# Optimization experiments

Measured on AMD Instinct MI355X. Metric: run time of the kernel, lower is better.

Reference implementation:

```python
import jax, jax.numpy as jnp
import numpy as np

B, S, D = 4, 2048, 1024
H = 16
HD = D // H

def setup_inputs() -> dict:
    key = jax.random.key(0)
    ks = jax.random.split(key, 6)
    scale = 1.0 / np.sqrt(D)
    x = jax.random.normal(ks[0], (B, S, D), dtype=jnp.float32)
    Wq = jax.random.normal(ks[1], (D, D), dtype=jnp.float32) * scale
    Wk = jax.random.normal(ks[2], (D, D), dtype=jnp.float32) * scale
    Wv = jax.random.normal(ks[3], (D, D), dtype=jnp.float32) * scale
    Wo = jax.random.normal(ks[4], (D, D), dtype=jnp.float32) * scale
    bo = jax.random.normal(ks[5], (D,), dtype=jnp.float32) * 0.01
    return {"x": x, "Wq": Wq, "Wk": Wk, "Wv": Wv, "Wo": Wo, "bo": bo}

def reference(x, Wq, Wk, Wv, Wo, bo):
    b, n, _ = x.shape
    # QKV projections (no bias), split into heads: [b, h, n, hd]
    q = (x @ Wq).reshape(b, n, H, HD).transpose(0, 2, 1, 3)
    k = (x @ Wk).reshape(b, n, H, HD).transpose(0, 2, 1, 3)
    v = (x @ Wv).reshape(b, n, H, HD).transpose(0, 2, 1, 3)
    scores = jnp.einsum('bhqd,bhkd->bhqk', q, k) / jnp.sqrt(jnp.float32(HD))
    causal = jnp.tril(jnp.ones((n, n), dtype=bool))
    scores = jnp.where(causal, scores, -jnp.inf)
    attn = jax.nn.softmax(scores, axis=-1)  # dropout p=0.0 -> identity
    ctx = jnp.einsum('bhqk,bhkd->bhqd', attn, v)
    ctx = ctx.transpose(0, 2, 1, 3).reshape(b, n, D)
    return ctx @ Wo + bo
```

## Files before the change

### kernel.cpp

```cpp
#include <hip/hip_runtime.h>

#define S_   2048
#define D_   1024
#define H_   16
#define HD_  64
#define NTOK 8192
#define QKS  2048
#define QSCALE 0.18033688f

typedef __attribute__((ext_vector_type(8))) __bf16 bf16x8;
typedef __attribute__((ext_vector_type(4))) __bf16 bf16x4;
typedef __attribute__((ext_vector_type(4))) float  f32x4;
typedef __attribute__((ext_vector_type(4))) short  short4v;

#define GPTR(p) ((__attribute__((address_space(1))) void*)(unsigned long long)(p))
#define LPTR(p) ((__attribute__((address_space(3))) void*)(p))

__global__ __launch_bounds__(256) void k_prep(const float* __restrict__ x,
                                              __bf16* __restrict__ xb,
                                              const float* __restrict__ Wq,
                                              const float* __restrict__ Wk,
                                              const float* __restrict__ Wv,
                                              const float* __restrict__ Wo,
                                              __bf16* __restrict__ wqkt,
                                              __bf16* __restrict__ wvt,
                                              __bf16* __restrict__ wot) {
    const int bx = blockIdx.x;
    if (bx < 4096) {
        int i = bx * 2048 + threadIdx.x * 8;
        f32x4 a = *(const f32x4*)(x + i);
        f32x4 b = *(const f32x4*)(x + i + 4);
        bf16x8 o;
#pragma unroll
        for (int j = 0; j < 4; j++) { o[j] = (__bf16)a[j]; o[4 + j] = (__bf16)b[j]; }
        *(bf16x8*)(xb + i) = o;
        return;
    }
    __shared__ float t[32][33];
    const int tt = bx - 4096;
    const int widx = tt >> 10, r = tt & 1023;
    const float* W;
    __bf16* Wt;
    switch (widx) {
        case 0: W = Wq; Wt = wqkt; break;
        case 1: W = Wk; Wt = wqkt + (size_t)D_ * D_; break;
        case 2: W = Wv; Wt = wvt; break;
        default: W = Wo; Wt = wot; break;
    }
    const int i0 = (r & 31) * 32, j0 = (r >> 5) * 32;
    const int tx = threadIdx.x & 31, ty = threadIdx.x >> 5;
#pragma unroll
    for (int rr = 0; rr < 32; rr += 8)
        t[ty + rr][tx] = W[(size_t)(i0 + ty + rr) * D_ + j0 + tx];
    __syncthreads();
#pragma unroll
    for (int rr = 0; rr < 32; rr += 8)
        Wt[(size_t)(j0 + ty + rr) * D_ + i0 + tx] = (__bf16)t[tx][ty + rr];
}

__device__ __forceinline__ void gemm_body_bf16(const __bf16* __restrict__ A,
                                               const __bf16* __restrict__ Bt,
                                               __bf16* __restrict__ C,
                                               int N, int K, int tm, int tn,
                                               float scale, int vperm,
                                               __bf16* As, __bf16* Bs) {
    const int tid  = threadIdx.x;
    const int wave = tid >> 6, lane = tid & 63;
    const int quad = lane >> 4, l16 = lane & 15;
    const int wm = (wave & 1) * 64, wn = (wave >> 1) * 64;
    f32x4 acc[4][4] = {};

    for (int k0 = 0; k0 < K; k0 += 32) {
        __syncthreads();
#pragma unroll
        for (int s = 0; s < 2; s++) {
            const int cb = s * 256 + wave * 64;
            const int c  = cb + lane;
            const int row = c >> 2;
            const int kc  = ((c & 3) ^ ((row >> 1) & 3)) * 8;
            __builtin_amdgcn_global_load_lds(GPTR(A + (size_t)(tm + row) * K + k0 + kc),
                                             LPTR(As + cb * 8), 16, 0, 0);
            __builtin_amdgcn_global_load_lds(GPTR(Bt + (size_t)(tn + row) * K + k0 + kc),
                                             LPTR(Bs + cb * 8), 16, 0, 0);
        }
        __syncthreads();

        bf16x8 af[4], bf[4];
#pragma unroll
        for (int mi = 0; mi < 4; mi++) {
            const int rf = wm + mi * 16 + l16;
            af[mi] = *(const bf16x8*)&As[rf * 32 + (quad ^ ((rf >> 1) & 3)) * 8];
        }
#pragma unroll
        for (int ni = 0; ni < 4; ni++) {
            const int rf = wn + ni * 16 + l16;
            bf[ni] = *(const bf16x8*)&Bs[rf * 32 + (quad ^ ((rf >> 1) & 3)) * 8];
        }
#pragma unroll
        for (int mi = 0; mi < 4; mi++)
#pragma unroll
            for (int ni = 0; ni < 4; ni++)
                acc[mi][ni] = __builtin_amdgcn_mfma_f32_16x16x32_bf16(
                    af[mi], bf[ni], acc[mi][ni], 0, 0, 0);
    }

#pragma unroll
    for (int mi = 0; mi < 4; mi++)
#pragma unroll
        for (int ni = 0; ni < 4; ni++)
#pragma unroll
            for (int r = 0; r < 4; r++) {
                const int row = tm + wm + mi * 16 + quad * 4 + r;
                const int col = tn + wn + ni * 16 + l16;
                const int xr  = (vperm & (row >> 3) & 1) << 2;
                C[(size_t)row * N + (col ^ xr)] = (__bf16)(acc[mi][ni][r] * scale);
            }
}

__global__ __launch_bounds__(256) void k_gemm_qkv(const __bf16* __restrict__ xb,
                                                  const __bf16* __restrict__ wqkt,
                                                  const __bf16* __restrict__ wvt,
                                                  __bf16* __restrict__ qk,
                                                  __bf16* __restrict__ VT) {
    __shared__ __bf16 As[128 * 32];
    __shared__ __bf16 Bs[128 * 32];
    const int bx = blockIdx.x;
    if (bx < 1024) {
        const int tm = (bx & 63) * 128, tn = (bx >> 6) * 128;
        const float scale = (tn < D_) ? QSCALE : 1.0f;
        gemm_body_bf16(xb, wqkt, qk, QKS, D_, tm, tn, scale, 0, As, Bs);
    } else {
        const int b2 = bx - 1024;
        const int tn = (b2 & 63) * 128, tm = (b2 >> 6) * 128;
        gemm_body_bf16(wvt, xb, VT, NTOK, D_, tm, tn, 1.0f, 1, As, Bs);
    }
}

__global__ __launch_bounds__(256) void k_gemm_o(const __bf16* __restrict__ A,
                                                const __bf16* __restrict__ Bt,
                                                float* __restrict__ C,
                                                const float* __restrict__ bias) {
    __shared__ __bf16 As[128 * 32];
    __shared__ __bf16 Bs[128 * 32];
    const int tid  = threadIdx.x;
    const int wave = tid >> 6, lane = tid & 63;
    const int quad = lane >> 4, l16 = lane & 15;
    const int tm = blockIdx.x * 128, tn = blockIdx.y * 128;
    const int wm = (wave & 1) * 64, wn = (wave >> 1) * 64;
    const int N = D_, K = D_;
    f32x4 acc[4][4] = {};

    for (int k0 = 0; k0 < K; k0 += 32) {
        __syncthreads();
#pragma unroll
        for (int s = 0; s < 2; s++) {
            const int cb = s * 256 + wave * 64;
            const int c  = cb + lane;
            const int row = c >> 2;
            const int kc  = ((c & 3) ^ ((row >> 1) & 3)) * 8;
            __builtin_amdgcn_global_load_lds(GPTR(A + (size_t)(tm + row) * K + k0 + kc),
                                             LPTR(As + cb * 8), 16, 0, 0);
            __builtin_amdgcn_global_load_lds(GPTR(Bt + (size_t)(tn + row) * K + k0 + kc),
                                             LPTR(Bs + cb * 8), 16, 0, 0);
        }
        __syncthreads();

        bf16x8 af[4], bf[4];
#pragma unroll
        for (int mi = 0; mi < 4; mi++) {
            const int rf = wm + mi * 16 + l16;
            af[mi] = *(const bf16x8*)&As[rf * 32 + (quad ^ ((rf >> 1) & 3)) * 8];
        }
#pragma unroll
        for (int ni = 0; ni < 4; ni++) {
            const int rf = wn + ni * 16 + l16;
            bf[ni] = *(const bf16x8*)&Bs[rf * 32 + (quad ^ ((rf >> 1) & 3)) * 8];
        }
#pragma unroll
        for (int mi = 0; mi < 4; mi++)
#pragma unroll
            for (int ni = 0; ni < 4; ni++)
                acc[mi][ni] = __builtin_amdgcn_mfma_f32_16x16x32_bf16(
                    af[mi], bf[ni], acc[mi][ni], 0, 0, 0);
    }

#pragma unroll
    for (int mi = 0; mi < 4; mi++)
#pragma unroll
        for (int ni = 0; ni < 4; ni++)
#pragma unroll
            for (int r = 0; r < 4; r++) {
                const int row = tm + wm + mi * 16 + quad * 4 + r;
                const int col = tn + wn + ni * 16 + l16;
                C[(size_t)row * N + col] = acc[mi][ni][r] + bias[col];
            }
}

__device__ __forceinline__ short bf16_bits(float f) {
    __bf16 h = (__bf16)f;
    return __builtin_bit_cast(short, h);
}

__global__ __launch_bounds__(256, 2) void k_attn(const __bf16* __restrict__ Qb,
                                                 const __bf16* __restrict__ Kb,
                                                 const __bf16* __restrict__ VT,
                                                 __bf16* __restrict__ ctx) {
    __shared__ __bf16 Ks[2][64 * 64];
    __shared__ __bf16 Vs[2][64 * 64];

    const int tid = threadIdx.x;
    const int wave = tid >> 6, lane = tid & 63;
    const int quad = lane >> 4, l16 = lane & 15;
    const int bid = blockIdx.x;
    const int hb  = ((bid >> 6) << 3) | (bid & 7);
    const int qp  = (bid >> 3) & 7;
    const int h = hb >> 2, b = hb & 3;
    const size_t tok0 = (size_t)b * S_;
    const size_t hoff = (size_t)h * HD_;

    auto stage = [&](int kv, int buf) {
#pragma unroll
        for (int s = 0; s < 2; s++) {
            const int cb = s * 256 + wave * 64;
            const int c  = cb + lane;
            const int row = c >> 3;
            const int gc  = (c & 7) ^ (row & 7);
            __builtin_amdgcn_global_load_lds(
                GPTR(Kb + (size_t)(tok0 + kv + row) * QKS + hoff + gc * 8),
                LPTR(&Ks[buf][cb * 8]), 16, 0, 0);
            __builtin_amdgcn_global_load_lds(
                GPTR(VT + (hoff + row) * (size_t)NTOK + tok0 + kv + gc * 8),
                LPTR(&Vs[buf][cb * 8]), 16, 0, 0);
        }
    };

#pragma unroll 1
    for (int sidx = 0; sidx < 2; sidx++) {
        const int qt = sidx == 0 ? qp : 15 - qp;
        const int qb = qt * 128;
        const int q0 = qb + wave * 32;

        bf16x8 qf[2][2];
#pragma unroll
        for (int qi = 0; qi < 2; qi++)
#pragma unroll
            for (int ks = 0; ks < 2; ks++)
                qf[qi][ks] = *(const bf16x8*)&Qb[(tok0 + q0 + qi * 16 + l16) * QKS +
                                                 hoff + ks * 32 + quad * 8];

        f32x4 oacc[2][4] = {};
        float lsum[2] = {0.f, 0.f};
        const int ktb = (qb + 127) >> 6;

        stage(0, 0);
        __syncthreads();

        for (int kt = 0; kt <= ktb; kt++) {
            const int cur = kt & 1;
            const int kv0 = kt * 64;
            if (kt < ktb) stage(kv0 + 64, 1 - cur);

            if (kv0 <= q0 + 31) {
                f32x4 st[2][4] = {};
#pragma unroll
                for (int ks = 0; ks < 2; ks++)
#pragma unroll
                    for (int ksub = 0; ksub < 4; ksub++) {
                        const int r = ksub * 16 + l16;
                        bf16x8 kf = *(const bf16x8*)
                            &Ks[cur][(r * 8 + (((ks * 4 + quad) ^ (r & 7)))) * 8];
#pragma unroll
                        for (int qi = 0; qi < 2; qi++)
                            st[qi][ksub] = __builtin_amdgcn_mfma_f32_16x16x32_bf16(
                                kf, qf[qi][ks], st[qi][ksub], 0, 0, 0);
                    }
                if (kv0 + 63 > q0) {
#pragma unroll
                    for (int qi = 0; qi < 2; qi++)
#pragma unroll
                        for (int ksub = 0; ksub < 4; ksub++)
#pragma unroll
                            for (int r = 0; r < 4; r++) {
                                const int kg = kv0 + ksub * 16 + quad * 4 + r;
                                const int qg = q0 + qi * 16 + l16;
                                if (kg > qg) st[qi][ksub][r] = -1e30f;
                            }
                }
                short4v pfrag[2][4];
#pragma unroll
                for (int qi = 0; qi < 2; qi++)
#pragma unroll
                    for (int ksub = 0; ksub < 4; ksub++) {
                        float p0 = __builtin_amdgcn_exp2f(st[qi][ksub][0]);
                        float p1 = __builtin_amdgcn_exp2f(st[qi][ksub][1]);
                        float p2 = __builtin_amdgcn_exp2f(st[qi][ksub][2]);
                        float p3 = __builtin_amdgcn_exp2f(st[qi][ksub][3]);
                        lsum[qi] += (p0 + p1) + (p2 + p3);
                        short4v pf = {bf16_bits(p0), bf16_bits(p1),
                                      bf16_bits(p2), bf16_bits(p3)};
                        pfrag[qi][ksub] = pf;
                    }
#pragma unroll
                for (int ksub = 0; ksub < 4; ksub++)
#pragma unroll
                    for (int hs = 0; hs < 4; hs++) {
                        const int row = hs * 16 + l16;
                        const int swz = (ksub * 2 + (quad >> 1)) ^ (row & 7);
                        short4v vf = *(const short4v*)
                            &Vs[cur][row * 64 + swz * 8 + ((quad ^ (l16 >> 3)) & 1) * 4];
#pragma unroll
                        for (int qi = 0; qi < 2; qi++)
                            oacc[qi][hs] = __builtin_amdgcn_mfma_f32_16x16x16bf16_1k(
                                vf, pfrag[qi][ksub], oacc[qi][hs], 0, 0, 0);
                    }
            }
            __syncthreads();
        }

#pragma unroll
        for (int qi = 0; qi < 2; qi++) {
            float v = lsum[qi];
            v += __shfl_xor(v, 16);
            v += __shfl_xor(v, 32);
            const float rl = 1.0f / v;
#pragma unroll
            for (int hs = 0; hs < 4; hs++) {
                bf16x4 o;
#pragma unroll
                for (int r = 0; r < 4; r++) o[r] = (__bf16)(oacc[qi][hs][r] * rl);
                *(bf16x4*)&ctx[(tok0 + q0 + qi * 16 + l16) * D_ + hoff +
                               hs * 16 + quad * 4] = o;
            }
        }
    }
}

extern "C" void kernel_launch(void* const* d_in, const int* in_sizes, int n_in,
                              void* d_out, int out_size, void* d_ws, size_t ws_size,
                              hipStream_t stream) {
    const float* x  = (const float*)d_in[0];
    const float* Wq = (const float*)d_in[1];
    const float* Wk = (const float*)d_in[2];
    const float* Wv = (const float*)d_in[3];
    const float* Wo = (const float*)d_in[4];
    const float* bo = (const float*)d_in[5];
    float* out = (float*)d_out;

    char* p = (char*)d_ws;
    __bf16* xb   = (__bf16*)p; p += (size_t)NTOK * D_ * 2;
    __bf16* wqkt = (__bf16*)p; p += (size_t)2 * D_ * D_ * 2;
    __bf16* wvt  = (__bf16*)p; p += (size_t)D_ * D_ * 2;
    __bf16* wot  = (__bf16*)p; p += (size_t)D_ * D_ * 2;
    __bf16* qk   = (__bf16*)p; p += (size_t)NTOK * QKS * 2;
    __bf16* VT   = (__bf16*)p; p += (size_t)NTOK * D_ * 2;
    __bf16* ctx  = (__bf16*)p; p += (size_t)NTOK * D_ * 2;

    k_prep<<<dim3(4096 + 4 * 1024), 256, 0, stream>>>(x, xb, Wq, Wk, Wv, Wo,
                                                      wqkt, wvt, wot);
    k_gemm_qkv<<<dim3(1024 + 512), 256, 0, stream>>>(xb, wqkt, wvt, qk, VT);
    k_attn<<<dim3(512), 256, 0, stream>>>(qk, qk + D_, VT, ctx);
    k_gemm_o<<<dim3(64, 8), 256, 0, stream>>>(ctx, wot, out, bo);
}
```

Baseline: 232.1 us.

## Shrink attention query tile to 64 rows and double grid with occupancy 4

```diff
diff --git a/kernel.cpp b/kernel.cpp
--- a/kernel.cpp
+++ b/kernel.cpp
@@ -201,7 +201,7 @@
     return __builtin_bit_cast(short, h);
 }
 
-__global__ __launch_bounds__(256, 2) void k_attn(const __bf16* __restrict__ Qb,
+__global__ __launch_bounds__(256, 4) void k_attn(const __bf16* __restrict__ Qb,
                                                  const __bf16* __restrict__ Kb,
                                                  const __bf16* __restrict__ VT,
                                                  __bf16* __restrict__ ctx) {
@@ -212,8 +212,8 @@
     const int wave = tid >> 6, lane = tid & 63;
     const int quad = lane >> 4, l16 = lane & 15;
     const int bid = blockIdx.x;
-    const int hb  = ((bid >> 6) << 3) | (bid & 7);
-    const int qp  = (bid >> 3) & 7;
+    const int hb  = ((bid >> 7) << 3) | (bid & 7);
+    const int qp  = (bid >> 3) & 15;
     const int h = hb >> 2, b = hb & 3;
     const size_t tok0 = (size_t)b * S_;
     const size_t hoff = (size_t)h * HD_;
@@ -235,22 +235,20 @@
     };
 
 #pragma unroll 1
-    for (int sidx = 0; sidx < 2; sidx++) {
-        const int qt = sidx == 0 ? qp : 15 - qp;
-        const int qb = qt * 128;
-        const int q0 = qb + wave * 32;
-
-        bf16x8 qf[2][2];
-#pragma unroll
-        for (int qi = 0; qi < 2; qi++)
-#pragma unroll
-            for (int ks = 0; ks < 2; ks++)
-                qf[qi][ks] = *(const bf16x8*)&Qb[(tok0 + q0 + qi * 16 + l16) * QKS +
-                                                 hoff + ks * 32 + quad * 8];
-
-        f32x4 oacc[2][4] = {};
-        float lsum[2] = {0.f, 0.f};
-        const int ktb = (qb + 127) >> 6;
+    for (int pass = 0; pass < 2; pass++) {
+        const int j  = pass == 0 ? 31 - qp : qp;
+        const int qb = j * 64;
+        const int q0 = qb + wave * 16;
+
+        bf16x8 qf[2];
+#pragma unroll
+        for (int ks = 0; ks < 2; ks++)
+            qf[ks] = *(const bf16x8*)&Qb[(tok0 + q0 + l16) * QKS +
+                                         hoff + ks * 32 + quad * 8];
+
+        f32x4 oacc[4] = {};
+        float lsum = 0.f;
+        const int ktb = j;
 
         stage(0, 0);
         __syncthreads();
@@ -260,8 +258,8 @@
             const int kv0 = kt * 64;
             if (kt < ktb) stage(kv0 + 64, 1 - cur);
 
-            if (kv0 <= q0 + 31) {
-                f32x4 st[2][4] = {};
+            if (kv0 <= q0 + 15) {
+                f32x4 st[4] = {};
 #pragma unroll
                 for (int ks = 0; ks < 2; ks++)
 #pragma unroll
@@ -269,37 +267,31 @@
                         const int r = ksub * 16 + l16;
                         bf16x8 kf = *(const bf16x8*)
                             &Ks[cur][(r * 8 + (((ks * 4 + quad) ^ (r & 7)))) * 8];
-#pragma unroll
-                        for (int qi = 0; qi < 2; qi++)
-                            st[qi][ksub] = __builtin_amdgcn_mfma_f32_16x16x32_bf16(
-                                kf, qf[qi][ks], st[qi][ksub], 0, 0, 0);
+                        st[ksub] = __builtin_amdgcn_mfma_f32_16x16x32_bf16(
+                            kf, qf[ks], st[ksub], 0, 0, 0);
                     }
                 if (kv0 + 63 > q0) {
 #pragma unroll
-                    for (int qi = 0; qi < 2; qi++)
-#pragma unroll
-                        for (int ksub = 0; ksub < 4; ksub++)
-#pragma unroll
-                            for (int r = 0; r < 4; r++) {
-                                const int kg = kv0 + ksub * 16 + quad * 4 + r;
-                                const int qg = q0 + qi * 16 + l16;
-                                if (kg > qg) st[qi][ksub][r] = -1e30f;
-                            }
+                    for (int ksub = 0; ksub < 4; ksub++)
+#pragma unroll
+                        for (int r = 0; r < 4; r++) {
+                            const int kg = kv0 + ksub * 16 + quad * 4 + r;
+                            const int qg = q0 + l16;
+                            if (kg > qg) st[ksub][r] = -1e30f;
+                        }
                 }
-                short4v pfrag[2][4];
-#pragma unroll
-                for (int qi = 0; qi < 2; qi++)
-#pragma unroll
-                    for (int ksub = 0; ksub < 4; ksub++) {
-                        float p0 = __builtin_amdgcn_exp2f(st[qi][ksub][0]);
-                        float p1 = __builtin_amdgcn_exp2f(st[qi][ksub][1]);
-                        float p2 = __builtin_amdgcn_exp2f(st[qi][ksub][2]);
-                        float p3 = __builtin_amdgcn_exp2f(st[qi][ksub][3]);
-                        lsum[qi] += (p0 + p1) + (p2 + p3);
-                        short4v pf = {bf16_bits(p0), bf16_bits(p1),
-                                      bf16_bits(p2), bf16_bits(p3)};
-                        pfrag[qi][ksub] = pf;
-                    }
+                short4v pfrag[4];
+#pragma unroll
+                for (int ksub = 0; ksub < 4; ksub++) {
+                    float p0 = __builtin_amdgcn_exp2f(st[ksub][0]);
+                    float p1 = __builtin_amdgcn_exp2f(st[ksub][1]);
+                    float p2 = __builtin_amdgcn_exp2f(st[ksub][2]);
+                    float p3 = __builtin_amdgcn_exp2f(st[ksub][3]);
+                    lsum += (p0 + p1) + (p2 + p3);
+                    short4v pf = {bf16_bits(p0), bf16_bits(p1),
+                                  bf16_bits(p2), bf16_bits(p3)};
+                    pfrag[ksub] = pf;
+                }
 #pragma unroll
                 for (int ksub = 0; ksub < 4; ksub++)
 #pragma unroll
@@ -308,18 +300,15 @@
                         const int swz = (ksub * 2 + (quad >> 1)) ^ (row & 7);
                         short4v vf = *(const short4v*)
                             &Vs[cur][row * 64 + swz * 8 + ((quad ^ (l16 >> 3)) & 1) * 4];
-#pragma unroll
-                        for (int qi = 0; qi < 2; qi++)
-                            oacc[qi][hs] = __builtin_amdgcn_mfma_f32_16x16x16bf16_1k(
-                                vf, pfrag[qi][ksub], oacc[qi][hs], 0, 0, 0);
+                        oacc[hs] = __builtin_amdgcn_mfma_f32_16x16x16bf16_1k(
+                            vf, pfrag[ksub], oacc[hs], 0, 0, 0);
                     }
             }
             __syncthreads();
         }
 
-#pragma unroll
-        for (int qi = 0; qi < 2; qi++) {
-            float v = lsum[qi];
+        {
+            float v = lsum;
             v += __shfl_xor(v, 16);
             v += __shfl_xor(v, 32);
             const float rl = 1.0f / v;
@@ -327,8 +316,8 @@
             for (int hs = 0; hs < 4; hs++) {
                 bf16x4 o;
 #pragma unroll
-                for (int r = 0; r < 4; r++) o[r] = (__bf16)(oacc[qi][hs][r] * rl);
-                *(bf16x4*)&ctx[(tok0 + q0 + qi * 16 + l16) * D_ + hoff +
+                for (int r = 0; r < 4; r++) o[r] = (__bf16)(oacc[hs][r] * rl);
+                *(bf16x4*)&ctx[(tok0 + q0 + l16) * D_ + hoff +
                                hs * 16 + quad * 4] = o;
             }
         }
@@ -358,6 +347,6 @@
     k_prep<<<dim3(4096 + 4 * 1024), 256, 0, stream>>>(x, xb, Wq, Wk, Wv, Wo,
                                                       wqkt, wvt, wot);
     k_gemm_qkv<<<dim3(1024 + 512), 256, 0, stream>>>(xb, wqkt, wvt, qk, VT);
-    k_attn<<<dim3(512), 256, 0, stream>>>(qk, qk + D_, VT, ctx);
+    k_attn<<<dim3(1024), 256, 0, stream>>>(qk, qk + D_, VT, ctx);
     k_gemm_o<<<dim3(64, 8), 256, 0, stream>>>(ctx, wot, out, bo);
 }
```

Result: no change. 234.7 us (+1.1%).
